# Kernel optimization log

Measured on AMD Instinct MI355X. Metric: run time of the kernel, lower is better.

The kernel has to match this reference:

```python
import jax, jax.numpy as jnp
import numpy as np

B, T, C, H = 2, 2048, 1024, 16
HD = C // H  # head dim = 64


def setup_inputs() -> dict:
    key = jax.random.key(0)
    k1, k2, k3 = jax.random.split(key, 3)
    scale_in = 1.0 / np.sqrt(C)
    x = jax.random.normal(k1, (B, T, C), dtype=jnp.float32)
    w_qkv = jax.random.normal(k2, (C, 3 * C), dtype=jnp.float32) * scale_in
    b_qkv = jnp.zeros((3 * C,), dtype=jnp.float32)
    w_out = jax.random.normal(k3, (C, C), dtype=jnp.float32) * scale_in
    b_out = jnp.zeros((C,), dtype=jnp.float32)
    return {"x": x, "w_qkv": w_qkv, "b_qkv": b_qkv, "w_out": w_out, "b_out": b_out}


def reference(x, w_qkv, b_qkv, w_out, b_out):
    Bq, Tq, Cq = x.shape
    qkv = x @ w_qkv + b_qkv                       # [B,T,3C]
    q, k, v = jnp.split(qkv, 3, axis=-1)          # each [B,T,C]
    # [B,T,C] -> [B,H,T,HD]
    q = q.reshape(Bq, Tq, H, HD).transpose(0, 2, 1, 3)
    k = k.reshape(Bq, Tq, H, HD).transpose(0, 2, 1, 3)
    v = v.reshape(Bq, Tq, H, HD).transpose(0, 2, 1, 3)
    scale = 1.0 / np.sqrt(HD)
    scores = jnp.einsum("bhqd,bhkd->bhqk", q, k) * scale  # [B,H,T,T]
    causal = jnp.tril(jnp.ones((Tq, Tq), dtype=bool))
    scores = jnp.where(causal[None, None], scores, jnp.finfo(scores.dtype).min)
    attn = jax.nn.softmax(scores, axis=-1)
    y = jnp.einsum("bhqk,bhkd->bhqd", attn, v)    # [B,H,T,HD]
    y = y.transpose(0, 2, 1, 3).reshape(Bq, Tq, Cq)
    return y @ w_out + b_out
```

## Files before the change

### kernel.cpp

```cpp
#include <hip/hip_runtime.h>
#include <hip/hip_bf16.h>


#define B_ 2
#define T_ 2048
#define C_ 1024
#define H_ 16
#define HD_ 64
#define M_ (B_ * T_)
#define N3_ (3 * C_)
#define QK2_ 2048
#define QSCALE 0.18033688f

typedef __attribute__((ext_vector_type(8))) short short8;
typedef __attribute__((ext_vector_type(4))) short short4v;
typedef __attribute__((ext_vector_type(4))) float floatx4;

__device__ __forceinline__ unsigned short f2b(float f) {
    __hip_bfloat16 h = __float2bfloat16(f);
    return *reinterpret_cast<unsigned short*>(&h);
}

__device__ __forceinline__ void glds16(const void* g, void* l) {
    __builtin_amdgcn_global_load_lds(
        (const __attribute__((address_space(1))) void*)g,
        (__attribute__((address_space(3))) void*)l, 16, 0, 0);
}

__global__ __launch_bounds__(256) void prep(
    const float* __restrict__ x, const float* __restrict__ w_qkv,
    const float* __restrict__ w_out, unsigned short* __restrict__ xb,
    unsigned short* __restrict__ wt1, unsigned short* __restrict__ wt2) {
    __shared__ float t[64][33];
    const int bi = blockIdx.x;
    const int tid = threadIdx.x;
    if (bi < 4096) {
        int i = (bi * 256 + tid) * 4;
        float4 v = *reinterpret_cast<const float4*>(x + i);
        short4v s;
        s[0] = (short)f2b(v.x); s[1] = (short)f2b(v.y);
        s[2] = (short)f2b(v.z); s[3] = (short)f2b(v.w);
        *reinterpret_cast<short4v*>(xb + i) = s;
        return;
    }
    const float* src; unsigned short* dst; int n0, k0, N;
    if (bi < 4096 + 1536) {
        int u = bi - 4096;
        src = w_qkv; dst = wt1; N = N3_;
        k0 = (u & 15) * 64; n0 = (u >> 4) * 32;
    } else {
        int u = bi - (4096 + 1536);
        src = w_out; dst = wt2; N = C_;
        k0 = (u & 15) * 64; n0 = (u >> 4) * 32;
    }
    const int tx = tid & 31, ty = tid >> 5;
#pragma unroll
    for (int i = 0; i < 8; i++)
        t[ty + i * 8][tx] = src[(size_t)(k0 + ty + i * 8) * N + n0 + tx];
    __syncthreads();
    const int row = tid >> 3;
    const int kp  = (tid & 7) * 8;
    short8 o;
#pragma unroll
    for (int j = 0; j < 8; j++) o[j] = (short)f2b(t[kp + j][row]);
    *reinterpret_cast<short8*>(&dst[(size_t)(n0 + row) * C_ + k0 + kp]) = o;
}

template<int EPI, int BN>
__global__ __launch_bounds__(256) void gemm_glds(
    const unsigned short* __restrict__ A, const unsigned short* __restrict__ Bt,
    const float* __restrict__ bias, void* __restrict__ Cp,
    unsigned short* __restrict__ vtp, int M, int N, int K) {
    constexpr int NI = BN / 32;
    __shared__ __align__(16) unsigned short Al[128 * 64];
    __shared__ __align__(16) unsigned short Bl[BN * 64];

    const int tid  = threadIdx.x;
    const int lane = tid & 63;
    const int w    = tid >> 6;
    const int c16  = lane & 15;
    const int quad = lane >> 4;
    const int NT  = N / BN;
    const int pe  = NT >> 3;
    const int xcd = blockIdx.x & 7;
    const int ii  = blockIdx.x >> 3;
    const int n0  = (xcd * pe + ii % pe) * BN;
    const int m0  = (ii / pe) * 128;
    const int wm = (w >> 1) * 64;
    const int wn = (w & 1) * (BN / 2);

    floatx4 acc[4][NI] = {};

    const int srow = lane >> 3;
    const int sch  = ((lane & 7) ^ srow) * 8;
    const unsigned short* ag = A + (size_t)(m0 + w * 32 + srow) * K + sch;
    const unsigned short* bg = Bt + (size_t)(n0 + w * (BN / 4) + srow) * K + sch;

    const int s7 = c16 & 7;

    for (int k0 = 0; k0 < K; k0 += 64) {
        __syncthreads();
#pragma unroll
        for (int i = 0; i < 4; i++)
            glds16(ag + k0 + (size_t)(i * 8) * K, &Al[(w * 32 + i * 8) * 64]);
#pragma unroll
        for (int i = 0; i < BN / 32; i++)
            glds16(bg + k0 + (size_t)(i * 8) * K,
                   &Bl[(w * (BN / 4) + i * 8) * 64]);
        __syncthreads();

        short8 af[4][2], bf[NI][2];
#pragma unroll
        for (int im = 0; im < 4; im++)
#pragma unroll
            for (int kk = 0; kk < 2; kk++)
                af[im][kk] = *reinterpret_cast<const short8*>(
                    &Al[(wm + im * 16 + c16) * 64 + ((kk * 4 + quad) ^ s7) * 8]);
#pragma unroll
        for (int in = 0; in < NI; in++)
#pragma unroll
            for (int kk = 0; kk < 2; kk++)
                bf[in][kk] = *reinterpret_cast<const short8*>(
                    &Bl[(wn + in * 16 + c16) * 64 + ((kk * 4 + quad) ^ s7) * 8]);
#pragma unroll
        for (int im = 0; im < 4; im++)
#pragma unroll
            for (int in = 0; in < NI; in++)
#pragma unroll
                for (int kk = 0; kk < 2; kk++)
                    acc[im][in] = __builtin_amdgcn_mfma_f32_16x16x32_bf16(
                        af[im][kk], bf[in][kk], acc[im][in], 0, 0, 0);
    }

    const int ncol = n0 + wn;
    float bv[NI];
#pragma unroll
    for (int in = 0; in < NI; in++) bv[in] = bias[ncol + in * 16 + c16];

    if (EPI == 0) {
        float* C = (float*)Cp;
#pragma unroll
        for (int im = 0; im < 4; im++)
#pragma unroll
            for (int r = 0; r < 4; r++) {
                int row = m0 + wm + im * 16 + quad * 4 + r;
#pragma unroll
                for (int in = 0; in < NI; in++)
                    C[(size_t)row * N + ncol + in * 16 + c16] =
                        acc[im][in][r] + bv[in];
            }
    } else {
        if (ncol < 2 * C_) {
            const float fac = (ncol < C_) ? QSCALE : 1.0f;
            unsigned short* qkp = (unsigned short*)Cp;
#pragma unroll
            for (int im = 0; im < 4; im++)
#pragma unroll
                for (int r = 0; r < 4; r++) {
                    int row = m0 + wm + im * 16 + quad * 4 + r;
#pragma unroll
                    for (int in = 0; in < NI; in++)
                        qkp[(size_t)row * QK2_ + ncol + in * 16 + c16] =
                            f2b((acc[im][in][r] + bv[in]) * fac);
                }
        } else {
#pragma unroll
            for (int im = 0; im < 4; im++) {
                int row0 = m0 + wm + im * 16 + quad * 4;
                int b  = row0 >> 11;
                int t0 = row0 & (T_ - 1);
#pragma unroll
                for (int in = 0; in < NI; in++) {
                    int dfull = ncol - 2 * C_ + in * 16 + c16;
                    short4v sv;
#pragma unroll
                    for (int r = 0; r < 4; r++)
                        sv[r] = (short)f2b(acc[im][in][r] + bv[in]);
                    *reinterpret_cast<short4v*>(
                        &vtp[(((size_t)(b << 10) + dfull) << 11) + t0]) = sv;
                }
            }
        }
    }
}

template<bool MASKED>
__device__ __forceinline__ void attn_tile(
    short8 af0, short8 af1,
    const unsigned short* __restrict__ Kb,
    const unsigned short* __restrict__ Vb,
    unsigned short* __restrict__ pw,
    floatx4 O[4], float& l,
    int row0, int kb, int c16, int quad) {
    const floatx4 z = {0.f, 0.f, 0.f, 0.f};
    const int sx  = c16 & 7;
    const int ch0 = (quad ^ sx) * 8;
    const int ch1 = ((quad + 4) ^ sx) * 8;
    floatx4 s[4];
#pragma unroll
    for (int nt = 0; nt < 4; nt++) {
        const int rb = (nt * 16 + c16) * 64;
        short8 k0 = *reinterpret_cast<const short8*>(&Kb[rb + ch0]);
        short8 k1 = *reinterpret_cast<const short8*>(&Kb[rb + ch1]);
        floatx4 t = __builtin_amdgcn_mfma_f32_16x16x32_bf16(k0, af0, z, 0, 0, 0);
        s[nt] = __builtin_amdgcn_mfma_f32_16x16x32_bf16(k1, af1, t, 0, 0, 0);
    }
    const int qrow = row0 + c16;
#pragma unroll
    for (int nt = 0; nt < 4; nt++) {
        short4v p4;
#pragma unroll
        for (int r = 0; r < 4; r++) {
            float p;
            if (MASKED) {
                int key = kb + nt * 16 + quad * 4 + r;
                p = (key <= qrow) ? exp2f(s[nt][r]) : 0.f;
            } else {
                p = exp2f(s[nt][r]);
            }
            l += p;
            p4[r] = (short)f2b(p);
        }
        const int pst = ((2 * nt + (quad >> 1)) ^ sx) * 8 + (quad & 1) * 4;
        *reinterpret_cast<short4v*>(&pw[c16 * 64 + pst]) = p4;
    }
    short8 pf0 = *reinterpret_cast<const short8*>(&pw[c16 * 64 + ch0]);
    short8 pf1 = *reinterpret_cast<const short8*>(&pw[c16 * 64 + ch1]);
#pragma unroll
    for (int nt = 0; nt < 4; nt++) {
        const int rb = (nt * 16 + c16) * 64;
        short8 v0 = *reinterpret_cast<const short8*>(&Vb[rb + ch0]);
        short8 v1 = *reinterpret_cast<const short8*>(&Vb[rb + ch1]);
        floatx4 t = __builtin_amdgcn_mfma_f32_16x16x32_bf16(pf0, v0, O[nt], 0, 0, 0);
        O[nt] = __builtin_amdgcn_mfma_f32_16x16x32_bf16(pf1, v1, t, 0, 0, 0);
    }
}

__global__ __launch_bounds__(256) void attn_mfma(
    const unsigned short* __restrict__ qk,
    const unsigned short* __restrict__ vt,
    unsigned short* __restrict__ y) {
    __shared__ __align__(16) unsigned short Kl[2][64 * 64];
    __shared__ __align__(16) unsigned short Vl[2][64 * 64];
    __shared__ __align__(16) unsigned short Pl[4 * 16 * 64];

    const int tid  = threadIdx.x;
    const int lane = tid & 63;
    const int w    = tid >> 6;
    const int c16  = lane & 15;
    const int quad = lane >> 4;
    const int bh = blockIdx.x & 31;
    const int t  = 31 - (blockIdx.x >> 5);
    const int b  = bh >> 4;
    const int h  = bh & 15;
    const int row0 = (4 * t + w) * 16;
    const int nch  = t + 1;

    const unsigned short* qrow = qk + (size_t)b * T_ * QK2_ + h * HD_;
    const unsigned short* krow = qrow + C_;
    const unsigned short* vrow = vt + ((size_t)bh << 6) * T_;

    short8 af0 = *reinterpret_cast<const short8*>(
        qrow + (size_t)(row0 + c16) * QK2_ + quad * 8);
    short8 af1 = *reinterpret_cast<const short8*>(
        qrow + (size_t)(row0 + c16) * QK2_ + 32 + quad * 8);

    floatx4 O[4] = {};
    float l = 0.f;
    unsigned short* pw = &Pl[w * 16 * 64];

    const int r8 = lane >> 3;
    const int sw = ((lane & 7) ^ r8) * 8;

#pragma unroll
    for (int i = 0; i < 2; i++) {
        const int row = w * 16 + i * 8 + r8;
        glds16(krow + (size_t)row * QK2_ + sw, &Kl[0][(w * 16 + i * 8) * 64]);
        glds16(vrow + (size_t)row * T_ + sw,   &Vl[0][(w * 16 + i * 8) * 64]);
    }

    for (int c = 0; c < nch; c++) {
        __syncthreads();
        if (c + 1 < nch) {
            const int kb2 = (c + 1) * 64;
            const int nb = (c + 1) & 1;
#pragma unroll
            for (int i = 0; i < 2; i++) {
                const int row = w * 16 + i * 8 + r8;
                glds16(krow + (size_t)(kb2 + row) * QK2_ + sw,
                       &Kl[nb][(w * 16 + i * 8) * 64]);
                glds16(vrow + (size_t)row * T_ + kb2 + sw,
                       &Vl[nb][(w * 16 + i * 8) * 64]);
            }
        }
        const int kb = c * 64;
        if (c + 1 < nch)
            attn_tile<false>(af0, af1, Kl[c & 1], Vl[c & 1], pw, O, l,
                             row0, kb, c16, quad);
        else
            attn_tile<true>(af0, af1, Kl[c & 1], Vl[c & 1], pw, O, l,
                            row0, kb, c16, quad);
    }

    l += __shfl_xor(l, 16);
    l += __shfl_xor(l, 32);
    float lr[4];
#pragma unroll
    for (int r = 0; r < 4; r++)
        lr[r] = __shfl(l, quad * 4 + r);

#pragma unroll
    for (int nt = 0; nt < 4; nt++)
#pragma unroll
        for (int r = 0; r < 4; r++) {
            float val = O[nt][r] / fmaxf(lr[r], 1e-30f);
            y[((size_t)b * T_ + row0 + quad * 4 + r) * C_ + h * HD_ + nt * 16 + c16] =
                f2b(val);
        }
}

extern "C" void kernel_launch(void* const* d_in, const int* in_sizes, int n_in,
                              void* d_out, int out_size, void* d_ws, size_t ws_size,
                              hipStream_t stream) {
    const float* x     = (const float*)d_in[0];
    const float* w_qkv = (const float*)d_in[1];
    const float* b_qkv = (const float*)d_in[2];
    const float* w_out = (const float*)d_in[3];
    const float* b_out = (const float*)d_in[4];
    float* out = (float*)d_out;

    unsigned short* qkb = (unsigned short*)d_ws;
    unsigned short* vtb = qkb + (size_t)M_ * QK2_;
    unsigned short* yb  = vtb + (size_t)B_ * H_ * HD_ * T_;
    unsigned short* wt1 = yb + (size_t)M_ * C_;
    unsigned short* wt2 = wt1 + (size_t)N3_ * C_;
    unsigned short* xb  = wt2 + (size_t)C_ * C_;

    prep<<<4096 + 1536 + 512, 256, 0, stream>>>(x, w_qkv, w_out, xb, wt1, wt2);

    gemm_glds<1, 128><<<(N3_ / 128) * (M_ / 128), 256, 0, stream>>>(
        xb, wt1, b_qkv, qkb, vtb, M_, N3_, C_);

    attn_mfma<<<B_ * H_ * 32, 256, 0, stream>>>(qkb, vtb, yb);

    gemm_glds<0, 64><<<(C_ / 64) * (M_ / 128), 256, 0, stream>>>(
        yb, wt2, b_out, out, nullptr, M_, C_, C_);
}
```

Baseline: 179.6 us.

## Split attention KV chunks across two wave groups with an LDS reduction

Doubles the attention block to 512 threads (8 waves). Each group of four waves handles alternating KV chunks, and every wave now issues one row of K and V async loads per chunk instead of two. At the end, group 1 writes its partial O and row sums to LDS and group 0 adds them and writes the output. The P scratch buffer is shared by both groups and a block-wide barrier still separates every chunk, so only one group computes per iteration. The change therefore mainly halves per-wave load work, at the cost of idle waves, more barrier participants and an extra reduction step.

```diff
diff --git a/kernel.cpp b/kernel.cpp
--- a/kernel.cpp
+++ b/kernel.cpp
@@ -236,7 +236,7 @@
     }
 }
 
-__global__ __launch_bounds__(256) void attn_mfma(
+__global__ __launch_bounds__(512) void attn_mfma(
     const unsigned short* __restrict__ qk,
     const unsigned short* __restrict__ vt,
     unsigned short* __restrict__ y) {
@@ -247,13 +247,15 @@
     const int tid  = threadIdx.x;
     const int lane = tid & 63;
     const int w    = tid >> 6;
+    const int wq   = w & 3;
+    const int par  = w >> 2;
     const int c16  = lane & 15;
     const int quad = lane >> 4;
     const int bh = blockIdx.x & 31;
     const int t  = 31 - (blockIdx.x >> 5);
     const int b  = bh >> 4;
     const int h  = bh & 15;
-    const int row0 = (4 * t + w) * 16;
+    const int row0 = (4 * t + wq) * 16;
     const int nch  = t + 1;
 
     const unsigned short* qrow = qk + (size_t)b * T_ * QK2_ + h * HD_;
@@ -267,56 +269,67 @@
 
     floatx4 O[4] = {};
     float l = 0.f;
-    unsigned short* pw = &Pl[w * 16 * 64];
+    unsigned short* pw = &Pl[wq * 16 * 64];
 
     const int r8 = lane >> 3;
     const int sw = ((lane & 7) ^ r8) * 8;
-
-#pragma unroll
-    for (int i = 0; i < 2; i++) {
-        const int row = w * 16 + i * 8 + r8;
-        glds16(krow + (size_t)row * QK2_ + sw, &Kl[0][(w * 16 + i * 8) * 64]);
-        glds16(vrow + (size_t)row * T_ + sw,   &Vl[0][(w * 16 + i * 8) * 64]);
-    }
+    const int srow = w * 8 + r8;
+
+    glds16(krow + (size_t)srow * QK2_ + sw, &Kl[0][(w * 8) * 64]);
+    glds16(vrow + (size_t)srow * T_ + sw,   &Vl[0][(w * 8) * 64]);
 
     for (int c = 0; c < nch; c++) {
         __syncthreads();
         if (c + 1 < nch) {
             const int kb2 = (c + 1) * 64;
             const int nb = (c + 1) & 1;
-#pragma unroll
-            for (int i = 0; i < 2; i++) {
-                const int row = w * 16 + i * 8 + r8;
-                glds16(krow + (size_t)(kb2 + row) * QK2_ + sw,
-                       &Kl[nb][(w * 16 + i * 8) * 64]);
-                glds16(vrow + (size_t)row * T_ + kb2 + sw,
-                       &Vl[nb][(w * 16 + i * 8) * 64]);
+            glds16(krow + (size_t)(kb2 + srow) * QK2_ + sw, &Kl[nb][(w * 8) * 64]);
+            glds16(vrow + (size_t)srow * T_ + kb2 + sw,     &Vl[nb][(w * 8) * 64]);
+        }
+        if ((c & 1) == par) {
+            const int kb = c * 64;
+            if (c + 1 < nch)
+                attn_tile<false>(af0, af1, Kl[c & 1], Vl[c & 1], pw, O, l,
+                                 row0, kb, c16, quad);
+            else
+                attn_tile<true>(af0, af1, Kl[c & 1], Vl[c & 1], pw, O, l,
+                                row0, kb, c16, quad);
+        }
+    }
+
+    __syncthreads();
+    float* Kf = (float*)&Kl[0][0];
+    float* Vf = (float*)&Vl[0][0];
+    if (par) {
+#pragma unroll
+        for (int nt = 0; nt < 4; nt++)
+            *reinterpret_cast<floatx4*>(&Kf[wq * 1024 + lane * 16 + nt * 4]) = O[nt];
+        Vf[wq * 64 + lane] = l;
+    }
+    __syncthreads();
+    if (par == 0) {
+#pragma unroll
+        for (int nt = 0; nt < 4; nt++)
+            O[nt] += *reinterpret_cast<const floatx4*>(
+                &Kf[wq * 1024 + lane * 16 + nt * 4]);
+        l += Vf[wq * 64 + lane];
+
+        l += __shfl_xor(l, 16);
+        l += __shfl_xor(l, 32);
+        float lr[4];
+#pragma unroll
+        for (int r = 0; r < 4; r++)
+            lr[r] = __shfl(l, quad * 4 + r);
+
+#pragma unroll
+        for (int nt = 0; nt < 4; nt++)
+#pragma unroll
+            for (int r = 0; r < 4; r++) {
+                float val = O[nt][r] / fmaxf(lr[r], 1e-30f);
+                y[((size_t)b * T_ + row0 + quad * 4 + r) * C_ + h * HD_ +
+                  nt * 16 + c16] = f2b(val);
             }
-        }
-        const int kb = c * 64;
-        if (c + 1 < nch)
-            attn_tile<false>(af0, af1, Kl[c & 1], Vl[c & 1], pw, O, l,
-                             row0, kb, c16, quad);
-        else
-            attn_tile<true>(af0, af1, Kl[c & 1], Vl[c & 1], pw, O, l,
-                            row0, kb, c16, quad);
-    }
-
-    l += __shfl_xor(l, 16);
-    l += __shfl_xor(l, 32);
-    float lr[4];
-#pragma unroll
-    for (int r = 0; r < 4; r++)
-        lr[r] = __shfl(l, quad * 4 + r);
-
-#pragma unroll
-    for (int nt = 0; nt < 4; nt++)
-#pragma unroll
-        for (int r = 0; r < 4; r++) {
-            float val = O[nt][r] / fmaxf(lr[r], 1e-30f);
-            y[((size_t)b * T_ + row0 + quad * 4 + r) * C_ + h * HD_ + nt * 16 + c16] =
-                f2b(val);
-        }
+    }
 }
 
 extern "C" void kernel_launch(void* const* d_in, const int* in_sizes, int n_in,
@@ -341,7 +354,7 @@
     gemm_glds<1, 128><<<(N3_ / 128) * (M_ / 128), 256, 0, stream>>>(
         xb, wt1, b_qkv, qkb, vtb, M_, N3_, C_);
 
-    attn_mfma<<<B_ * H_ * 32, 256, 0, stream>>>(qkb, vtb, yb);
+    attn_mfma<<<B_ * H_ * 32, 512, 0, stream>>>(qkb, vtb, yb);
 
     gemm_glds<0, 64><<<(C_ / 64) * (M_ / 128), 256, 0, stream>>>(
         yb, wt2, b_out, out, nullptr, M_, C_, C_);
```

Measured after the change: 175.5 us. -2.3%, faster.

## Double attention block to 128 query rows with eight waves sharing K/V tiles

Applied to the files above, without the earlier changes.

The attention kernel now uses 512 threads (8 waves) per block covering 128 query rows, so each staged K/V chunk in shared memory is reused by twice as many waves. This halves the number of blocks and the global K/V traffic per query row. Block ordering changes to interleave long and short causal tiles, and waves in the lower half skip the last chunk they do not need. The cost is fewer blocks in the grid, idle waves at the diagonal chunk, and more barrier participants per step.

```diff
diff --git a/kernel.cpp b/kernel.cpp
--- a/kernel.cpp
+++ b/kernel.cpp
@@ -236,13 +236,13 @@
     }
 }
 
-__global__ __launch_bounds__(256) void attn_mfma(
+__global__ __launch_bounds__(512) void attn_mfma(
     const unsigned short* __restrict__ qk,
     const unsigned short* __restrict__ vt,
     unsigned short* __restrict__ y) {
     __shared__ __align__(16) unsigned short Kl[2][64 * 64];
     __shared__ __align__(16) unsigned short Vl[2][64 * 64];
-    __shared__ __align__(16) unsigned short Pl[4 * 16 * 64];
+    __shared__ __align__(16) unsigned short Pl[8 * 16 * 64];
 
     const int tid  = threadIdx.x;
     const int lane = tid & 63;
@@ -250,11 +250,13 @@
     const int c16  = lane & 15;
     const int quad = lane >> 4;
     const int bh = blockIdx.x & 31;
-    const int t  = 31 - (blockIdx.x >> 5);
+    const int tg = blockIdx.x >> 5;
+    const int t  = (tg < 8) ? (15 - tg) : (tg - 8);
     const int b  = bh >> 4;
     const int h  = bh & 15;
-    const int row0 = (4 * t + w) * 16;
-    const int nch  = t + 1;
+    const int row0 = (8 * t + w) * 16;
+    const int nch_w   = 2 * t + (w >> 2) + 1;
+    const int nch_max = 2 * t + 2;
 
     const unsigned short* qrow = qk + (size_t)b * T_ * QK2_ + h * HD_;
     const unsigned short* krow = qrow + C_;
@@ -271,35 +273,28 @@
 
     const int r8 = lane >> 3;
     const int sw = ((lane & 7) ^ r8) * 8;
-
-#pragma unroll
-    for (int i = 0; i < 2; i++) {
-        const int row = w * 16 + i * 8 + r8;
-        glds16(krow + (size_t)row * QK2_ + sw, &Kl[0][(w * 16 + i * 8) * 64]);
-        glds16(vrow + (size_t)row * T_ + sw,   &Vl[0][(w * 16 + i * 8) * 64]);
-    }
-
-    for (int c = 0; c < nch; c++) {
+    const int srow = w * 8 + r8;
+
+    glds16(krow + (size_t)srow * QK2_ + sw, &Kl[0][(w * 8) * 64]);
+    glds16(vrow + (size_t)srow * T_ + sw,   &Vl[0][(w * 8) * 64]);
+
+    for (int c = 0; c < nch_max; c++) {
         __syncthreads();
-        if (c + 1 < nch) {
+        if (c + 1 < nch_max) {
             const int kb2 = (c + 1) * 64;
             const int nb = (c + 1) & 1;
-#pragma unroll
-            for (int i = 0; i < 2; i++) {
-                const int row = w * 16 + i * 8 + r8;
-                glds16(krow + (size_t)(kb2 + row) * QK2_ + sw,
-                       &Kl[nb][(w * 16 + i * 8) * 64]);
-                glds16(vrow + (size_t)row * T_ + kb2 + sw,
-                       &Vl[nb][(w * 16 + i * 8) * 64]);
-            }
-        }
-        const int kb = c * 64;
-        if (c + 1 < nch)
-            attn_tile<false>(af0, af1, Kl[c & 1], Vl[c & 1], pw, O, l,
-                             row0, kb, c16, quad);
-        else
-            attn_tile<true>(af0, af1, Kl[c & 1], Vl[c & 1], pw, O, l,
-                            row0, kb, c16, quad);
+            glds16(krow + (size_t)(kb2 + srow) * QK2_ + sw, &Kl[nb][(w * 8) * 64]);
+            glds16(vrow + (size_t)srow * T_ + kb2 + sw,     &Vl[nb][(w * 8) * 64]);
+        }
+        if (c < nch_w) {
+            const int kb = c * 64;
+            if (c + 1 < nch_w)
+                attn_tile<false>(af0, af1, Kl[c & 1], Vl[c & 1], pw, O, l,
+                                 row0, kb, c16, quad);
+            else
+                attn_tile<true>(af0, af1, Kl[c & 1], Vl[c & 1], pw, O, l,
+                                row0, kb, c16, quad);
+        }
     }
 
     l += __shfl_xor(l, 16);
@@ -341,7 +336,7 @@
     gemm_glds<1, 128><<<(N3_ / 128) * (M_ / 128), 256, 0, stream>>>(
         xb, wt1, b_qkv, qkb, vtb, M_, N3_, C_);
 
-    attn_mfma<<<B_ * H_ * 32, 256, 0, stream>>>(qkb, vtb, yb);
+    attn_mfma<<<32 * 16, 512, 0, stream>>>(qkb, vtb, yb);
 
     gemm_glds<0, 64><<<(C_ / 64) * (M_ / 128), 256, 0, stream>>>(
         yb, wt2, b_out, out, nullptr, M_, C_, C_);
```

Result: slower. 184.6 us (+2.8%).
